# Kernel tuning notes

Hardware: AMD Instinct MI355X
Metric: run time of the kernel (lower is better)

Reference implementation:

```python
import jax, jax.numpy as jnp
import numpy as np

EMBED_DIM = 2048
NUM_HEADS = 16
HEAD_DIM = EMBED_DIM // NUM_HEADS
BATCH = 4
SEQ = 1024
ROPE_BASE = 10000.0


def _rotate_half(x):
    x1, x2 = jnp.split(x, 2, axis=-1)
    return jnp.concatenate([-x2, x1], axis=-1)


def setup_inputs() -> dict:
    key = jax.random.key(0)
    ks = jax.random.split(key, 8)
    query = jax.random.normal(ks[0], (BATCH, SEQ, EMBED_DIM), dtype=jnp.float32)
    kkey = jax.random.normal(ks[1], (BATCH, SEQ, EMBED_DIM), dtype=jnp.float32)
    value = jax.random.normal(ks[2], (BATCH, SEQ, EMBED_DIM), dtype=jnp.float32)
    # causal mask: scores.masked_fill(mask == 0, -inf)
    mask = jnp.tril(jnp.ones((SEQ, SEQ), dtype=jnp.int32))[None, None]
    # RoPE tables [S, head_dim]
    inv_freq = 1.0 / (ROPE_BASE ** (np.arange(0, HEAD_DIM, 2, dtype=np.float32) / HEAD_DIM))
    pos = np.arange(SEQ, dtype=np.float32)
    freqs = np.outer(pos, inv_freq)                      # [S, D/2]
    emb = np.concatenate([freqs, freqs], axis=-1)        # [S, D]
    rope_cos = jnp.asarray(np.cos(emb), dtype=jnp.float32)
    rope_sin = jnp.asarray(np.sin(emb), dtype=jnp.float32)
    s = 1.0 / np.sqrt(EMBED_DIM)
    Wq = jax.random.normal(ks[3], (EMBED_DIM, EMBED_DIM), dtype=jnp.float32) * s
    Wk = jax.random.normal(ks[4], (EMBED_DIM, EMBED_DIM), dtype=jnp.float32) * s
    Wv = jax.random.normal(ks[5], (EMBED_DIM, EMBED_DIM), dtype=jnp.float32) * s
    Wo = jax.random.normal(ks[6], (EMBED_DIM, EMBED_DIM), dtype=jnp.float32) * s
    return {"query": query, "key": kkey, "value": value, "mask": mask,
            "rope_cos": rope_cos, "rope_sin": rope_sin,
            "Wq": Wq, "Wk": Wk, "Wv": Wv, "Wo": Wo}


def reference(query, key, value, mask, rope_cos, rope_sin, Wq, Wk, Wv, Wo):
    B, S, E = query.shape
    # projections (nn.Linear: x @ W.T)
    def proj(x, W):
        y = x @ W.T
        return y.reshape(B, -1, NUM_HEADS, HEAD_DIM).transpose(0, 2, 1, 3)  # [B,H,S,D]
    Q = proj(query, Wq)
    K = proj(key, Wk)
    V = proj(value, Wv)
    # RoPE (rotate-half form), cos/sin broadcast over batch and heads
    cos = rope_cos[None, None]  # [1,1,S,D]
    sin = rope_sin[None, None]
    Q = Q * cos + _rotate_half(Q) * sin
    K = K * cos + _rotate_half(K) * sin
    scale = jnp.asarray(np.sqrt(HEAD_DIM), dtype=Q.dtype)
    scores = jnp.einsum('bhqd,bhkd->bhqk', Q, K) / scale
    scores = jnp.where(mask == 0, jnp.asarray(-jnp.inf, scores.dtype), scores)
    attn = jax.nn.softmax(scores, axis=-1)
    context = jnp.einsum('bhqk,bhkd->bhqd', attn, V)
    context = context.transpose(0, 2, 1, 3).reshape(B, S, E)
    out = context @ Wo.T
    return out
```

## Files before the change

### kernel.cpp

```cpp
#include <hip/hip_runtime.h>
#include <stdint.h>

#define E_DIM 2048
#define N_HEADS 16
#define H_DIM 128
#define BATCH 4
#define SEQL 1024
#define M_ROWS 4096

typedef __attribute__((ext_vector_type(8))) short bf16x8;
typedef __attribute__((ext_vector_type(4))) float f32x4;

#define AS1 __attribute__((address_space(1)))
#define AS3 __attribute__((address_space(3)))

__device__ __forceinline__ void gload16(const void* g, void* l) {
  __builtin_amdgcn_global_load_lds((const AS1 uint32_t*)g, (AS3 uint32_t*)l, 16, 0, 0);
}

__device__ __forceinline__ unsigned short f2bf(float f) {
  union { float f; uint32_t u; } v; v.f = f;
  return (unsigned short)((v.u + 0x7FFFu + ((v.u >> 16) & 1u)) >> 16);
}

__global__ __launch_bounds__(256) void k_cvtx(const float* __restrict__ a,
                                              const float* __restrict__ b,
                                              const float* __restrict__ c,
                                              ushort* __restrict__ oa,
                                              ushort* __restrict__ ob,
                                              ushort* __restrict__ oc) {
  int which = blockIdx.y;
  const float* in = (which == 0) ? a : (which == 1) ? b : c;
  ushort* out = (which == 0) ? oa : (which == 1) ? ob : oc;
  int i = (blockIdx.x * 256 + threadIdx.x) * 4;
  float4 v = *reinterpret_cast<const float4*>(in + i);
  *reinterpret_cast<ushort4*>(out + i) =
      make_ushort4(f2bf(v.x), f2bf(v.y), f2bf(v.z), f2bf(v.w));
}

__global__ __launch_bounds__(256) void k_cvtw(const float* __restrict__ a,
                                              const float* __restrict__ b,
                                              const float* __restrict__ c,
                                              const float* __restrict__ d,
                                              ushort* __restrict__ oa,
                                              ushort* __restrict__ ob,
                                              ushort* __restrict__ oc,
                                              ushort* __restrict__ od) {
  int which = blockIdx.y;
  const float* in = (which == 0) ? a : (which == 1) ? b : (which == 2) ? c : d;
  ushort* out = (which == 0) ? oa : (which == 1) ? ob : (which == 2) ? oc : od;
  int i = (blockIdx.x * 256 + threadIdx.x) * 4;
  float4 v = *reinterpret_cast<const float4*>(in + i);
  *reinterpret_cast<ushort4*>(out + i) =
      make_ushort4(f2bf(v.x), f2bf(v.y), f2bf(v.z), f2bf(v.w));
}

__device__ __forceinline__ void gemm256_mainloop(const ushort* __restrict__ A,
                                                 const ushort* __restrict__ W,
                                                 ushort* lds, int m0, int n0,
                                                 const int browRows[4],
                                                 f32x4 (&acc)[8][4]) {
  const int tid = threadIdx.x;
  const int w = tid >> 6, lane = tid & 63, quad = lane >> 4, lid = lane & 15;

  ushort* bufA[2] = {lds, lds + 16384};
  ushort* bufB[2] = {lds + 32768, lds + 49152};

  const int p0 = tid, p1i = tid + 512;
  const int r0 = p0 >> 3, c0 = (p0 & 7) ^ (r0 & 7);
  const int r1 = p1i >> 3, c1 = (p1i & 7) ^ (r1 & 7);
  const int ld0 = (w * 64) * 8;
  const int ld1 = (512 + w * 64) * 8;

  const ushort* gA = A + (size_t)m0 * E_DIM;
  const ushort* gB = W + (size_t)n0 * E_DIM;

  auto stage = [&](const ushort* g, ushort* buf, int kt, int half) {
    const ushort* s0p = g + (size_t)(half * 128 + r0) * E_DIM + kt * 64 + c0 * 8;
    const ushort* s1p = g + (size_t)(half * 128 + r1) * E_DIM + kt * 64 + c1 * 8;
    ushort* l = buf + half * 8192;
    gload16(s0p, l + ld0);
    gload16(s1p, l + ld1);
  };

  int ofsA[2], ofsB[4][2];
  {
    const int rowA = (w >> 2) * 128 + lid;
#pragma unroll
    for (int ks = 0; ks < 2; ++ks)
      ofsA[ks] = rowA * 64 + (((ks * 4 + quad) ^ (lid & 7)) * 8);
#pragma unroll
    for (int ni = 0; ni < 4; ++ni)
#pragma unroll
      for (int ks = 0; ks < 2; ++ks)
        ofsB[ni][ks] = browRows[ni] * 64 + (((ks * 4 + quad) ^ (lid & 7)) * 8);
  }

  bf16x8 bfr[4][2];

#define LDB(b)                                                                 \
  do {                                                                         \
    _Pragma("unroll") for (int ni = 0; ni < 4; ++ni)                           \
        _Pragma("unroll") for (int ks = 0; ks < 2; ++ks)                       \
            bfr[ni][ks] =                                                      \
                *reinterpret_cast<const bf16x8*>(bufB[b] + ofsB[ni][ks]);      \
  } while (0)

#define PH(b, q, STG, VMW)                                                     \
  do {                                                                         \
    bf16x8 af[2][2];                                                           \
    if ((q) == 0) LDB(b);                                                      \
    _Pragma("unroll") for (int d = 0; d < 2; ++d)                              \
        _Pragma("unroll") for (int ks = 0; ks < 2; ++ks)                       \
            af[d][ks] = *reinterpret_cast<const bf16x8*>(                      \
                bufA[b] + ofsA[ks] + ((q) * 2 + d) * 1024);                    \
    STG;                                                                       \
    VMW;                                                                       \
    __builtin_amdgcn_s_barrier();                                              \
    asm volatile("s_waitcnt lgkmcnt(0)" ::: "memory");                         \
    __builtin_amdgcn_s_setprio(1);                                             \
    _Pragma("unroll") for (int ks = 0; ks < 2; ++ks)                           \
        _Pragma("unroll") for (int d = 0; d < 2; ++d)                          \
            _Pragma("unroll") for (int ni = 0; ni < 4; ++ni)                   \
                acc[(q) * 2 + d][ni] = __builtin_amdgcn_mfma_f32_16x16x32_bf16(\
                    af[d][ks], bfr[ni][ks], acc[(q) * 2 + d][ni], 0, 0, 0);    \
    __builtin_amdgcn_s_setprio(0);                                             \
    __builtin_amdgcn_s_barrier();                                              \
  } while (0)

  stage(gB, bufB[0], 0, 0); stage(gB, bufB[0], 0, 1);
  stage(gA, bufA[0], 0, 0); stage(gA, bufA[0], 0, 1);
  stage(gB, bufB[1], 1, 0); stage(gB, bufB[1], 1, 1);
  asm volatile("s_waitcnt vmcnt(4)" ::: "memory");
  __builtin_amdgcn_s_barrier();

  for (int i = 0; i < 16; ++i) {
    const bool lastI = (i == 15);
    const int tn = 2 * i;
    PH(0, 0, stage(gA, bufA[1], tn + 1, 0), );
    PH(0, 1, stage(gA, bufA[1], tn + 1, 1), );
    PH(0, 2, if (!lastI) stage(gB, bufB[0], tn + 2, 0), );
    PH(0, 3, if (!lastI) stage(gB, bufB[0], tn + 2, 1),
       if (lastI) asm volatile("s_waitcnt vmcnt(0)" ::: "memory");
       else asm volatile("s_waitcnt vmcnt(4)" ::: "memory"));
    PH(1, 0, if (!lastI) stage(gA, bufA[0], tn + 2, 0), );
    PH(1, 1, if (!lastI) stage(gA, bufA[0], tn + 2, 1), );
    PH(1, 2, if (!lastI) stage(gB, bufB[1], tn + 3, 0), );
    PH(1, 3, if (!lastI) stage(gB, bufB[1], tn + 3, 1),
       if (!lastI) asm volatile("s_waitcnt vmcnt(4)" ::: "memory"));
  }
#undef PH
#undef LDB
}

__global__ __launch_bounds__(512, 2) void k_gemm_qkv(
    const ushort* __restrict__ xq, const ushort* __restrict__ xk, const ushort* __restrict__ xv,
    const ushort* __restrict__ wq, const ushort* __restrict__ wk, const ushort* __restrict__ wv,
    ushort* __restrict__ Qr, ushort* __restrict__ Kr, ushort* __restrict__ Vr,
    const float* __restrict__ cosT, const float* __restrict__ sinT) {
  extern __shared__ ushort lds[];
  const int z = blockIdx.z;
  const ushort* A = (z == 0) ? xq : (z == 1) ? xk : xv;
  const ushort* W = (z == 0) ? wq : (z == 1) ? wk : wv;
  ushort* Out = (z == 0) ? Qr : (z == 1) ? Kr : Vr;
  const int tid = threadIdx.x;
  const int w = tid >> 6, lane = tid & 63, quad = lane >> 4, lid = lane & 15;
  const int wn = w & 3;
  const int n0 = blockIdx.x * 256;
  const int m0 = blockIdx.y * 256;

  int browRows[4];
#pragma unroll
  for (int ni = 0; ni < 4; ++ni)
    browRows[ni] = (wn >> 1) * 128 + (wn & 1) * 32 + (ni & 1) * 16 + (ni >> 1) * 64 + lid;

  f32x4 acc[8][4];
  const f32x4 z4 = {0.f, 0.f, 0.f, 0.f};
#pragma unroll
  for (int i = 0; i < 8; ++i)
#pragma unroll
    for (int j = 0; j < 4; ++j) acc[i][j] = z4;

  gemm256_mainloop(A, W, lds, m0, n0, browRows, acc);

  const int b = m0 >> 10;
  const int h = blockIdx.x * 2 + (wn >> 1);
  ushort* Og = Out + (size_t)(b * N_HEADS + h) * SEQL * H_DIM;
  const bool rope = (z < 2);
#pragma unroll
  for (int mi = 0; mi < 8; ++mi)
#pragma unroll
    for (int r = 0; r < 4; ++r) {
      int s = (m0 & (SEQL - 1)) + (w >> 2) * 128 + mi * 16 + quad * 4 + r;
      size_t row = (size_t)s * H_DIM;
      if (rope) {
#pragma unroll
        for (int ni = 0; ni < 2; ++ni) {
          int d0 = (wn & 1) * 32 + ni * 16 + lid;
          float c = cosT[s * H_DIM + d0];
          float sn = sinT[s * H_DIM + d0];
          float x0 = acc[mi][ni][r], x1 = acc[mi][ni + 2][r];
          Og[row + d0]      = f2bf(x0 * c - x1 * sn);
          Og[row + d0 + 64] = f2bf(x1 * c + x0 * sn);
        }
      } else {
#pragma unroll
        for (int ni = 0; ni < 4; ++ni) {
          int d = (wn & 1) * 32 + (ni & 1) * 16 + (ni >> 1) * 64 + lid;
          Og[row + d] = f2bf(acc[mi][ni][r]);
        }
      }
    }
}

__global__ __launch_bounds__(512, 2) void k_gemm_o(const ushort* __restrict__ A,
                                                   const ushort* __restrict__ W,
                                                   float* __restrict__ Out) {
  extern __shared__ ushort lds[];
  const int tid = threadIdx.x;
  const int w = tid >> 6, lane = tid & 63, quad = lane >> 4, lid = lane & 15;
  const int wn = w & 3;
  const int n0 = blockIdx.x * 256;
  const int m0 = blockIdx.y * 256;

  int browRows[4];
#pragma unroll
  for (int ni = 0; ni < 4; ++ni) browRows[ni] = wn * 64 + ni * 16 + lid;

  f32x4 acc[8][4];
  const f32x4 z4 = {0.f, 0.f, 0.f, 0.f};
#pragma unroll
  for (int i = 0; i < 8; ++i)
#pragma unroll
    for (int j = 0; j < 4; ++j) acc[i][j] = z4;

  gemm256_mainloop(A, W, lds, m0, n0, browRows, acc);

#pragma unroll
  for (int mi = 0; mi < 8; ++mi)
#pragma unroll
    for (int r = 0; r < 4; ++r) {
      size_t row = (size_t)(m0 + (w >> 2) * 128 + mi * 16 + quad * 4 + r) * E_DIM + n0;
#pragma unroll
      for (int ni = 0; ni < 4; ++ni) Out[row + browRows[ni]] = acc[mi][ni][r];
    }
}

__global__ __launch_bounds__(256) void k_transv(const ushort* __restrict__ V,
                                                ushort* __restrict__ Vt) {
  __shared__ ushort t[32][33];
  int bh = blockIdx.z;
  int s0 = blockIdx.x * 32;
  int d0 = blockIdx.y * 32;
  int j = threadIdx.x & 31;
  int i = threadIdx.x >> 5;
  for (int rr = 0; rr < 4; ++rr) {
    int row = i + rr * 8;
    t[row][j] = V[((size_t)bh * SEQL + s0 + row) * H_DIM + d0 + j];
  }
  __syncthreads();
  for (int rr = 0; rr < 4; ++rr) {
    int drow = i + rr * 8;
    Vt[((size_t)bh * H_DIM + d0 + drow) * SEQL + s0 + j] = t[j][drow];
  }
}

__global__ __launch_bounds__(256, 2) void k_attn(const ushort* __restrict__ Q,
                                                 const ushort* __restrict__ K,
                                                 const ushort* __restrict__ Vt,
                                                 ushort* __restrict__ Ctx) {
  __shared__ ushort Ks[128 * 128];
  __shared__ ushort Vs[128 * 64];
  __shared__ ushort Ps[4][32 * 40];
  const int tid = threadIdx.x;
  const int w = tid >> 6, lane = tid & 63, quad = lane >> 4, lid = lane & 15;
  const int l = blockIdx.y * 8 + blockIdx.x;
  const int bh = l & 63;
  const int slot = l >> 6;
  const int qt = (slot < 4) ? slot : 11 - slot;
  const int q0 = qt * 128;
  const size_t base = (size_t)bh * SEQL * H_DIM;
  const ushort* Qg = Q + base;
  const ushort* Kg = K + base;
  const ushort* Vg = Vt + base;

  bf16x8 qf[2][4];
  for (int mt = 0; mt < 2; ++mt) {
    int row = q0 + w * 32 + mt * 16 + lid;
    for (int kc = 0; kc < 4; ++kc)
      qf[mt][kc] = *reinterpret_cast<const bf16x8*>(Qg + (size_t)row * H_DIM + kc * 32 + quad * 8);
  }

  f32x4 oacc[2][8];
  f32x4 lacc[2];
  const f32x4 z4 = {0.f, 0.f, 0.f, 0.f};
  for (int mt = 0; mt < 2; ++mt) {
    lacc[mt] = z4;
    for (int dt = 0; dt < 8; ++dt) oacc[mt][dt] = z4;
  }

  bf16x8 ones;
  for (int i = 0; i < 8; ++i) ones[i] = (short)0x3F80;

  const float SC2 = 0.08838834764831845f * 1.4426950408889634f;
  const float M2 = 12.0f * 1.4426950408889634f;

  for (int j0 = 0; j0 <= q0; j0 += 128) {
    const bool diag = (j0 == q0);
    __syncthreads();
    for (int i = 0; i < 8; ++i) {
      int g = i * 256 + tid;
      int kk = g >> 4;
      int c = (g & 15) ^ (kk & 15);
      gload16(Kg + (size_t)(j0 + kk) * H_DIM + c * 8, Ks + (i * 256 + w * 64) * 8);
    }
    for (int i = 0; i < 4; ++i) {
      int g = i * 256 + tid;
      int d = g >> 3;
      int c = (g & 7) ^ (d & 7);
      gload16(Vg + (size_t)d * SEQL + j0 + c * 8, Vs + (i * 256 + w * 64) * 8);
    }
    __syncthreads();

    f32x4 sacc[2][8];
    for (int mt = 0; mt < 2; ++mt)
      for (int nt = 0; nt < 8; ++nt) sacc[mt][nt] = z4;
    for (int kc = 0; kc < 4; ++kc)
      for (int nt = 0; nt < 8; ++nt) {
        int kk = nt * 16 + lid;
        bf16x8 kf = *reinterpret_cast<const bf16x8*>(
            Ks + kk * H_DIM + (((kc * 4 + quad) ^ lid) * 8));
        sacc[0][nt] = __builtin_amdgcn_mfma_f32_16x16x32_bf16(qf[0][kc], kf, sacc[0][nt], 0, 0, 0);
        sacc[1][nt] = __builtin_amdgcn_mfma_f32_16x16x32_bf16(qf[1][kc], kf, sacc[1][nt], 0, 0, 0);
      }

    if (diag) {
      for (int mt = 0; mt < 2; ++mt)
        for (int nt = 0; nt < 8; ++nt)
          for (int r = 0; r < 4; ++r) {
            int key = j0 + nt * 16 + lid;
            int row = q0 + w * 32 + mt * 16 + quad * 4 + r;
            if (key > row) sacc[mt][nt][r] = -3.0e38f;
          }
    }

    ushort* Pw = Ps[w];
    for (int kc = 0; kc < 4; ++kc) {
      if (kc == 2) {
        __syncthreads();
        for (int i = 0; i < 4; ++i) {
          int g = i * 256 + tid;
          int d = g >> 3;
          int c = (g & 7) ^ (d & 7);
          gload16(Vg + (size_t)d * SEQL + j0 + 64 + c * 8, Vs + (i * 256 + w * 64) * 8);
        }
        __syncthreads();
      }
      for (int mt = 0; mt < 2; ++mt)
        for (int half = 0; half < 2; ++half) {
          int nt = kc * 2 + half;
          for (int r = 0; r < 4; ++r) {
            float p = exp2f(fmaf(sacc[mt][nt][r], SC2, -M2));
            Pw[(mt * 16 + quad * 4 + r) * 40 + half * 16 + lid] = f2bf(p);
          }
        }
      bf16x8 pf0 = *reinterpret_cast<const bf16x8*>(Pw + lid * 40 + quad * 8);
      bf16x8 pf1 = *reinterpret_cast<const bf16x8*>(Pw + (16 + lid) * 40 + quad * 8);
      lacc[0] = __builtin_amdgcn_mfma_f32_16x16x32_bf16(pf0, ones, lacc[0], 0, 0, 0);
      lacc[1] = __builtin_amdgcn_mfma_f32_16x16x32_bf16(pf1, ones, lacc[1], 0, 0, 0);
      int kcl = kc & 1;
      for (int dt = 0; dt < 8; ++dt) {
        int d = dt * 16 + lid;
        bf16x8 vf = *reinterpret_cast<const bf16x8*>(
            Vs + d * 64 + (((kcl * 4 + quad) ^ (d & 7)) * 8));
        oacc[0][dt] = __builtin_amdgcn_mfma_f32_16x16x32_bf16(pf0, vf, oacc[0][dt], 0, 0, 0);
        oacc[1][dt] = __builtin_amdgcn_mfma_f32_16x16x32_bf16(pf1, vf, oacc[1][dt], 0, 0, 0);
      }
    }
  }

  const int b = bh >> 4, h = bh & 15;
  for (int mt = 0; mt < 2; ++mt)
    for (int r = 0; r < 4; ++r) {
      int s = q0 + w * 32 + mt * 16 + quad * 4 + r;
      float inv = 1.0f / lacc[mt][r];
      for (int dt = 0; dt < 8; ++dt)
        Ctx[(size_t)(b * SEQL + s) * E_DIM + h * H_DIM + dt * 16 + lid] =
            f2bf(oacc[mt][dt][r] * inv);
    }
}

extern "C" void kernel_launch(void* const* d_in, const int* in_sizes, int n_in,
                              void* d_out, int out_size, void* d_ws, size_t ws_size,
                              hipStream_t stream) {
  const float* q_in = (const float*)d_in[0];
  const float* k_in = (const float*)d_in[1];
  const float* v_in = (const float*)d_in[2];
  const float* rc = (const float*)d_in[4];
  const float* rs = (const float*)d_in[5];
  const float* Wq = (const float*)d_in[6];
  const float* Wk = (const float*)d_in[7];
  const float* Wv = (const float*)d_in[8];
  const float* Wo = (const float*)d_in[9];
  float* out = (float*)d_out;

  ushort* p = (ushort*)d_ws;
  const size_t WSZ = (size_t)E_DIM * E_DIM;
  const size_t XSZ = (size_t)M_ROWS * E_DIM;
  ushort* wq_b = p; p += WSZ;
  ushort* wk_b = p; p += WSZ;
  ushort* wv_b = p; p += WSZ;
  ushort* wo_b = p; p += WSZ;
  ushort* xq_b = p; p += XSZ;
  ushort* xk_b = p; p += XSZ;
  ushort* xv_b = p; p += XSZ;
  ushort* Qr = p;   p += XSZ;
  ushort* Kr = p;   p += XSZ;
  ushort* Vr = p;   p += XSZ;
  ushort* Vt = p;   p += XSZ;
  ushort* ctx = xq_b;

  (void)hipFuncSetAttribute(reinterpret_cast<const void*>(k_gemm_qkv),
                            hipFuncAttributeMaxDynamicSharedMemorySize, 131072);
  (void)hipFuncSetAttribute(reinterpret_cast<const void*>(k_gemm_o),
                            hipFuncAttributeMaxDynamicSharedMemorySize, 131072);

  dim3 blk(256);
  k_cvtx<<<dim3((unsigned)(XSZ / 1024), 3), blk, 0, stream>>>(q_in, k_in, v_in, xq_b, xk_b, xv_b);
  k_cvtw<<<dim3((unsigned)(WSZ / 1024), 4), blk, 0, stream>>>(Wq, Wk, Wv, Wo, wq_b, wk_b, wv_b, wo_b);

  k_gemm_qkv<<<dim3(E_DIM / 256, M_ROWS / 256, 3), dim3(512), 131072, stream>>>(
      xq_b, xk_b, xv_b, wq_b, wk_b, wv_b, Qr, Kr, Vr, rc, rs);

  k_transv<<<dim3(SEQL / 32, H_DIM / 32, BATCH * N_HEADS), blk, 0, stream>>>(Vr, Vt);

  k_attn<<<dim3(8, BATCH * N_HEADS), blk, 0, stream>>>(Qr, Kr, Vt, ctx);

  k_gemm_o<<<dim3(E_DIM / 256, M_ROWS / 256), dim3(512), 131072, stream>>>(ctx, wo_b, out);
}
```

Baseline: 416.7 us.

## Triple-buffer GEMM A tiles, swizzle block order, narrow O-proj tiles, merge converts

The shared GEMM mainloop is rewritten to triple-buffer the A operand in LDS, with loads issued two k-tiles ahead. It is templated on the N-tile width so the output projection can use 256x128 tiles, doubling its block count to 256 for better CU fill. Both GEMMs remap block indices so that consecutive blocks share operand tiles for L2 reuse. The two fp32-to-bf16 conversion kernels are merged into one launch. QKV LDS use rises to 160KB, which probably limits that kernel to one block per CU, and the narrower O tiles lower arithmetic intensity.

```diff
diff --git a/kernel.cpp b/kernel.cpp
--- a/kernel.cpp
+++ b/kernel.cpp
@@ -23,134 +23,132 @@
   return (unsigned short)((v.u + 0x7FFFu + ((v.u >> 16) & 1u)) >> 16);
 }
 
-__global__ __launch_bounds__(256) void k_cvtx(const float* __restrict__ a,
-                                              const float* __restrict__ b,
-                                              const float* __restrict__ c,
-                                              ushort* __restrict__ oa,
-                                              ushort* __restrict__ ob,
-                                              ushort* __restrict__ oc) {
-  int which = blockIdx.y;
-  const float* in = (which == 0) ? a : (which == 1) ? b : c;
-  ushort* out = (which == 0) ? oa : (which == 1) ? ob : oc;
+__global__ __launch_bounds__(256) void k_cvt(
+    const float* __restrict__ q, const float* __restrict__ k, const float* __restrict__ v,
+    const float* __restrict__ wq, const float* __restrict__ wk,
+    const float* __restrict__ wv, const float* __restrict__ wo,
+    ushort* __restrict__ oq, ushort* __restrict__ ok, ushort* __restrict__ ov,
+    ushort* __restrict__ owq, ushort* __restrict__ owk,
+    ushort* __restrict__ owv, ushort* __restrict__ owo) {
+  int y = blockIdx.y;
+  const float* in;
+  ushort* out;
+  if (y < 3) {
+    in = (y == 0) ? q : (y == 1) ? k : v;
+    out = (y == 0) ? oq : (y == 1) ? ok : ov;
+  } else {
+    if (blockIdx.x >= 4096) return;
+    in = (y == 3) ? wq : (y == 4) ? wk : (y == 5) ? wv : wo;
+    out = (y == 3) ? owq : (y == 4) ? owk : (y == 5) ? owv : owo;
+  }
   int i = (blockIdx.x * 256 + threadIdx.x) * 4;
-  float4 v = *reinterpret_cast<const float4*>(in + i);
+  float4 vv = *reinterpret_cast<const float4*>(in + i);
   *reinterpret_cast<ushort4*>(out + i) =
-      make_ushort4(f2bf(v.x), f2bf(v.y), f2bf(v.z), f2bf(v.w));
-}
-
-__global__ __launch_bounds__(256) void k_cvtw(const float* __restrict__ a,
-                                              const float* __restrict__ b,
-                                              const float* __restrict__ c,
-                                              const float* __restrict__ d,
-                                              ushort* __restrict__ oa,
-                                              ushort* __restrict__ ob,
-                                              ushort* __restrict__ oc,
-                                              ushort* __restrict__ od) {
-  int which = blockIdx.y;
-  const float* in = (which == 0) ? a : (which == 1) ? b : (which == 2) ? c : d;
-  ushort* out = (which == 0) ? oa : (which == 1) ? ob : (which == 2) ? oc : od;
-  int i = (blockIdx.x * 256 + threadIdx.x) * 4;
-  float4 v = *reinterpret_cast<const float4*>(in + i);
-  *reinterpret_cast<ushort4*>(out + i) =
-      make_ushort4(f2bf(v.x), f2bf(v.y), f2bf(v.z), f2bf(v.w));
-}
-
+      make_ushort4(f2bf(vv.x), f2bf(vv.y), f2bf(vv.z), f2bf(vv.w));
+}
+
+template <int NREP>
 __device__ __forceinline__ void gemm256_mainloop(const ushort* __restrict__ A,
                                                  const ushort* __restrict__ W,
                                                  ushort* lds, int m0, int n0,
-                                                 const int browRows[4],
-                                                 f32x4 (&acc)[8][4]) {
+                                                 const int browRows[NREP],
+                                                 f32x4 (&acc)[8][NREP]) {
   const int tid = threadIdx.x;
   const int w = tid >> 6, lane = tid & 63, quad = lane >> 4, lid = lane & 15;
-
-  ushort* bufA[2] = {lds, lds + 16384};
-  ushort* bufB[2] = {lds + 32768, lds + 49152};
-
-  const int p0 = tid, p1i = tid + 512;
-  const int r0 = p0 >> 3, c0 = (p0 & 7) ^ (r0 & 7);
-  const int r1 = p1i >> 3, c1 = (p1i & 7) ^ (r1 & 7);
-  const int ld0 = (w * 64) * 8;
-  const int ld1 = (512 + w * 64) * 8;
-
-  const ushort* gA = A + (size_t)m0 * E_DIM;
-  const ushort* gB = W + (size_t)n0 * E_DIM;
-
-  auto stage = [&](const ushort* g, ushort* buf, int kt, int half) {
-    const ushort* s0p = g + (size_t)(half * 128 + r0) * E_DIM + kt * 64 + c0 * 8;
-    const ushort* s1p = g + (size_t)(half * 128 + r1) * E_DIM + kt * 64 + c1 * 8;
-    ushort* l = buf + half * 8192;
-    gload16(s0p, l + ld0);
-    gload16(s1p, l + ld1);
-  };
-
-  int ofsA[2], ofsB[4][2];
+  constexpr int KTILES = E_DIM / 64;
+  constexpr int BELE = NREP * 4096;
+  ushort* const bufA = lds;
+  ushort* const bufB = lds + 3 * 16384;
+
+  const int r0 = tid >> 3, c0 = (tid & 7) ^ (r0 & 7);
+  const int ldw = w * 512;
+  const ushort* aB = A + ((size_t)m0 + r0) * E_DIM + c0 * 8;
+  const ushort* bB = W + ((size_t)n0 + r0) * E_DIM + c0 * 8;
+
+#define STG(baseP, buf, kt, half)                                              \
+  do {                                                                         \
+    const ushort* _g = (baseP) + (size_t)(half) * 128 * E_DIM + (kt) * 64;     \
+    gload16(_g, (buf) + (half) * 8192 + ldw);                                  \
+    gload16(_g + (size_t)64 * E_DIM, (buf) + (half) * 8192 + 4096 + ldw);      \
+  } while (0)
+
+  int ofsA[2], ofsB[NREP][2];
   {
     const int rowA = (w >> 2) * 128 + lid;
 #pragma unroll
     for (int ks = 0; ks < 2; ++ks)
       ofsA[ks] = rowA * 64 + (((ks * 4 + quad) ^ (lid & 7)) * 8);
 #pragma unroll
-    for (int ni = 0; ni < 4; ++ni)
+    for (int ni = 0; ni < NREP; ++ni)
 #pragma unroll
       for (int ks = 0; ks < 2; ++ks)
         ofsB[ni][ks] = browRows[ni] * 64 + (((ks * 4 + quad) ^ (lid & 7)) * 8);
   }
 
-  bf16x8 bfr[4][2];
-
-#define LDB(b)                                                                 \
+  bf16x8 bfr[NREP][2];
+
+#define VMW_STEADY                                                             \
   do {                                                                         \
-    _Pragma("unroll") for (int ni = 0; ni < 4; ++ni)                           \
-        _Pragma("unroll") for (int ks = 0; ks < 2; ++ks)                       \
-            bfr[ni][ks] =                                                      \
-                *reinterpret_cast<const bf16x8*>(bufB[b] + ofsB[ni][ks]);      \
+    if constexpr (NREP == 4)                                                   \
+      asm volatile("s_waitcnt vmcnt(8)" ::: "memory");                         \
+    else                                                                       \
+      asm volatile("s_waitcnt vmcnt(6)" ::: "memory");                         \
   } while (0)
 
-#define PH(b, q, STG, VMW)                                                     \
+#define PH(aoff, boff, q, STGS, VMW)                                           \
   do {                                                                         \
     bf16x8 af[2][2];                                                           \
-    if ((q) == 0) LDB(b);                                                      \
+    if ((q) == 0) {                                                            \
+      _Pragma("unroll") for (int ni = 0; ni < NREP; ++ni)                      \
+          _Pragma("unroll") for (int ks = 0; ks < 2; ++ks)                     \
+              bfr[ni][ks] = *reinterpret_cast<const bf16x8*>(                  \
+                  bufB + (boff) + ofsB[ni][ks]);                               \
+    }                                                                          \
     _Pragma("unroll") for (int d = 0; d < 2; ++d)                              \
         _Pragma("unroll") for (int ks = 0; ks < 2; ++ks)                       \
             af[d][ks] = *reinterpret_cast<const bf16x8*>(                      \
-                bufA[b] + ofsA[ks] + ((q) * 2 + d) * 1024);                    \
-    STG;                                                                       \
+                bufA + (aoff) + ofsA[ks] + ((q) * 2 + d) * 1024);              \
+    STGS;                                                                      \
     VMW;                                                                       \
     __builtin_amdgcn_s_barrier();                                              \
     asm volatile("s_waitcnt lgkmcnt(0)" ::: "memory");                         \
     __builtin_amdgcn_s_setprio(1);                                             \
     _Pragma("unroll") for (int ks = 0; ks < 2; ++ks)                           \
         _Pragma("unroll") for (int d = 0; d < 2; ++d)                          \
-            _Pragma("unroll") for (int ni = 0; ni < 4; ++ni)                   \
+            _Pragma("unroll") for (int ni = 0; ni < NREP; ++ni)                \
                 acc[(q) * 2 + d][ni] = __builtin_amdgcn_mfma_f32_16x16x32_bf16(\
                     af[d][ks], bfr[ni][ks], acc[(q) * 2 + d][ni], 0, 0, 0);    \
     __builtin_amdgcn_s_setprio(0);                                             \
     __builtin_amdgcn_s_barrier();                                              \
   } while (0)
 
-  stage(gB, bufB[0], 0, 0); stage(gB, bufB[0], 0, 1);
-  stage(gA, bufA[0], 0, 0); stage(gA, bufA[0], 0, 1);
-  stage(gB, bufB[1], 1, 0); stage(gB, bufB[1], 1, 1);
-  asm volatile("s_waitcnt vmcnt(4)" ::: "memory");
+  STG(aB, bufA, 0, 0); STG(aB, bufA, 0, 1);
+  STG(bB, bufB, 0, 0); if (NREP == 4) STG(bB, bufB, 0, 1);
+  STG(aB, bufA + 16384, 1, 0); STG(aB, bufA + 16384, 1, 1);
+  STG(bB, bufB + BELE, 1, 0); if (NREP == 4) STG(bB, bufB + BELE, 1, 1);
+  VMW_STEADY;
   __builtin_amdgcn_s_barrier();
 
-  for (int i = 0; i < 16; ++i) {
-    const bool lastI = (i == 15);
-    const int tn = 2 * i;
-    PH(0, 0, stage(gA, bufA[1], tn + 1, 0), );
-    PH(0, 1, stage(gA, bufA[1], tn + 1, 1), );
-    PH(0, 2, if (!lastI) stage(gB, bufB[0], tn + 2, 0), );
-    PH(0, 3, if (!lastI) stage(gB, bufB[0], tn + 2, 1),
-       if (lastI) asm volatile("s_waitcnt vmcnt(0)" ::: "memory");
-       else asm volatile("s_waitcnt vmcnt(4)" ::: "memory"));
-    PH(1, 0, if (!lastI) stage(gA, bufA[0], tn + 2, 0), );
-    PH(1, 1, if (!lastI) stage(gA, bufA[0], tn + 2, 1), );
-    PH(1, 2, if (!lastI) stage(gB, bufB[1], tn + 3, 0), );
-    PH(1, 3, if (!lastI) stage(gB, bufB[1], tn + 3, 1),
-       if (!lastI) asm volatile("s_waitcnt vmcnt(4)" ::: "memory"));
+  int cur = 0, nx2 = 2;
+  for (int t = 0; t < KTILES; ++t) {
+    const int aoff = cur * 16384;
+    const int boff = (t & 1) * BELE;
+    ushort* sA = bufA + nx2 * 16384;
+    ushort* sB = bufB + boff;
+    const bool st = (t < KTILES - 2);
+    PH(aoff, boff, 0, if (st) STG(aB, sA, t + 2, 0), );
+    PH(aoff, boff, 1, if (st) STG(aB, sA, t + 2, 1), );
+    PH(aoff, boff, 2, if (st) STG(bB, sB, t + 2, 0), );
+    PH(aoff, boff, 3, if (st && NREP == 4) STG(bB, sB, t + 2, 1),
+       if (st) VMW_STEADY;
+       else if (t == KTILES - 2)
+           asm volatile("s_waitcnt vmcnt(0)" ::: "memory"));
+    cur = (cur == 2) ? 0 : cur + 1;
+    nx2 = (nx2 == 2) ? 0 : nx2 + 1;
   }
 #undef PH
-#undef LDB
+#undef VMW_STEADY
+#undef STG
 }
 
 __global__ __launch_bounds__(512, 2) void k_gemm_qkv(
@@ -159,15 +157,20 @@
     ushort* __restrict__ Qr, ushort* __restrict__ Kr, ushort* __restrict__ Vr,
     const float* __restrict__ cosT, const float* __restrict__ sinT) {
   extern __shared__ ushort lds[];
-  const int z = blockIdx.z;
+  unsigned lin = blockIdx.x + 8u * (blockIdx.y + 16u * blockIdx.z);
+  unsigned swz = (lin & 7u) * 48u + (lin >> 3);
+  const int bx = swz & 7u;
+  const int by = (swz >> 3) & 15u;
+  const int z = swz >> 7;
+
   const ushort* A = (z == 0) ? xq : (z == 1) ? xk : xv;
   const ushort* W = (z == 0) ? wq : (z == 1) ? wk : wv;
   ushort* Out = (z == 0) ? Qr : (z == 1) ? Kr : Vr;
   const int tid = threadIdx.x;
   const int w = tid >> 6, lane = tid & 63, quad = lane >> 4, lid = lane & 15;
   const int wn = w & 3;
-  const int n0 = blockIdx.x * 256;
-  const int m0 = blockIdx.y * 256;
+  const int n0 = bx * 256;
+  const int m0 = by * 256;
 
   int browRows[4];
 #pragma unroll
@@ -181,10 +184,10 @@
 #pragma unroll
     for (int j = 0; j < 4; ++j) acc[i][j] = z4;
 
-  gemm256_mainloop(A, W, lds, m0, n0, browRows, acc);
+  gemm256_mainloop<4>(A, W, lds, m0, n0, browRows, acc);
 
   const int b = m0 >> 10;
-  const int h = blockIdx.x * 2 + (wn >> 1);
+  const int h = bx * 2 + (wn >> 1);
   ushort* Og = Out + (size_t)(b * N_HEADS + h) * SEQL * H_DIM;
   const bool rope = (z < 2);
 #pragma unroll
@@ -217,24 +220,29 @@
                                                    const ushort* __restrict__ W,
                                                    float* __restrict__ Out) {
   extern __shared__ ushort lds[];
+  unsigned lin = blockIdx.x + 16u * blockIdx.y;
+  unsigned swz = (lin & 7u) * 32u + (lin >> 3);
+  const int bx = swz & 15u;
+  const int by = swz >> 4;
+
   const int tid = threadIdx.x;
   const int w = tid >> 6, lane = tid & 63, quad = lane >> 4, lid = lane & 15;
   const int wn = w & 3;
-  const int n0 = blockIdx.x * 256;
-  const int m0 = blockIdx.y * 256;
-
-  int browRows[4];
-#pragma unroll
-  for (int ni = 0; ni < 4; ++ni) browRows[ni] = wn * 64 + ni * 16 + lid;
-
-  f32x4 acc[8][4];
+  const int n0 = bx * 128;
+  const int m0 = by * 256;
+
+  int browRows[2];
+#pragma unroll
+  for (int ni = 0; ni < 2; ++ni) browRows[ni] = wn * 32 + ni * 16 + lid;
+
+  f32x4 acc[8][2];
   const f32x4 z4 = {0.f, 0.f, 0.f, 0.f};
 #pragma unroll
   for (int i = 0; i < 8; ++i)
 #pragma unroll
-    for (int j = 0; j < 4; ++j) acc[i][j] = z4;
-
-  gemm256_mainloop(A, W, lds, m0, n0, browRows, acc);
+    for (int j = 0; j < 2; ++j) acc[i][j] = z4;
+
+  gemm256_mainloop<2>(A, W, lds, m0, n0, browRows, acc);
 
 #pragma unroll
   for (int mi = 0; mi < 8; ++mi)
@@ -242,7 +250,7 @@
     for (int r = 0; r < 4; ++r) {
       size_t row = (size_t)(m0 + (w >> 2) * 128 + mi * 16 + quad * 4 + r) * E_DIM + n0;
 #pragma unroll
-      for (int ni = 0; ni < 4; ++ni) Out[row + browRows[ni]] = acc[mi][ni][r];
+      for (int ni = 0; ni < 2; ++ni) Out[row + browRows[ni]] = acc[mi][ni][r];
     }
 }
 
@@ -421,20 +429,20 @@
   ushort* ctx = xq_b;
 
   (void)hipFuncSetAttribute(reinterpret_cast<const void*>(k_gemm_qkv),
-                            hipFuncAttributeMaxDynamicSharedMemorySize, 131072);
+                            hipFuncAttributeMaxDynamicSharedMemorySize, 163840);
   (void)hipFuncSetAttribute(reinterpret_cast<const void*>(k_gemm_o),
                             hipFuncAttributeMaxDynamicSharedMemorySize, 131072);
 
   dim3 blk(256);
-  k_cvtx<<<dim3((unsigned)(XSZ / 1024), 3), blk, 0, stream>>>(q_in, k_in, v_in, xq_b, xk_b, xv_b);
-  k_cvtw<<<dim3((unsigned)(WSZ / 1024), 4), blk, 0, stream>>>(Wq, Wk, Wv, Wo, wq_b, wk_b, wv_b, wo_b);
-
-  k_gemm_qkv<<<dim3(E_DIM / 256, M_ROWS / 256, 3), dim3(512), 131072, stream>>>(
+  k_cvt<<<dim3(8192, 7), blk, 0, stream>>>(q_in, k_in, v_in, Wq, Wk, Wv, Wo,
+                                           xq_b, xk_b, xv_b, wq_b, wk_b, wv_b, wo_b);
+
+  k_gemm_qkv<<<dim3(E_DIM / 256, M_ROWS / 256, 3), dim3(512), 163840, stream>>>(
       xq_b, xk_b, xv_b, wq_b, wk_b, wv_b, Qr, Kr, Vr, rc, rs);
 
   k_transv<<<dim3(SEQL / 32, H_DIM / 32, BATCH * N_HEADS), blk, 0, stream>>>(Vr, Vt);
 
   k_attn<<<dim3(8, BATCH * N_HEADS), blk, 0, stream>>>(Qr, Kr, Vt, ctx);
 
-  k_gemm_o<<<dim3(E_DIM / 256, M_ROWS / 256), dim3(512), 131072, stream>>>(ctx, wo_b, out);
-}
+  k_gemm_o<<<dim3(E_DIM / 128, M_ROWS / 256), dim3(512), 131072, stream>>>(ctx, wo_b, out);
+}
```

After: 423.7 us. Within noise of the previous version (+1.7%).
